# Kernel tuning notes

Measured on AMD Instinct MI355X. Metric: run time of the kernel, lower is better.

## Reference

```python
import jax, jax.numpy as jnp
import numpy as np

N_POINTS = 262144
NUM_LEVELS = 16
LEVEL_DIM = 8
BASE_RES = 16
LOG2_HASH = 21
BOUNDS = 10.0
TEXT_REP = 512
IMAGE_REP = 512
MLP_WIDTH = 256
PRIMES = (1, 2654435761, 805459861)  # instant-NGP fast_hash primes


def _level_layout():
    # mirrors torch-ngp GridEncoder offset computation
    max_params = 2 ** LOG2_HASH
    sizes, offsets = [], [0]
    for l in range(NUM_LEVELS):
        res = int(np.ceil(BASE_RES * (2.0 ** l)))
        p = min(max_params, res ** 3)
        p = int(np.ceil(p / 8) * 8)  # align to 8
        sizes.append(p)
        offsets.append(offsets[-1] + p)
    return sizes, offsets

SIZES, OFFSETS = _level_layout()
TOTAL_PARAMS = OFFSETS[-1]  # ~27.56M rows


def grid_encode(u, embeddings):
    """u: [N,3] in [0,1]; torch-ngp kernel remaps with bound=1: u=(u+1)/2.
    With this config (res+1)^3 > hashmap_size at every level, so the hash
    path is always taken (faithful to get_grid_index)."""
    u = (u + 1.0) * 0.5
    feats = []
    for l in range(NUM_LEVELS):
        scale = 2.0 ** l * BASE_RES - 1.0          # exp2(l*log2(s))*H - 1
        pos = u * scale + 0.5                       # align_corners=False
        base = jnp.floor(pos)
        frac = pos - base                           # [N,3] trilinear fracs
        pg = base.astype(jnp.uint32)
        acc = jnp.zeros((u.shape[0], LEVEL_DIM), dtype=u.dtype)
        for corner in range(8):
            bits = [(corner >> d) & 1 for d in range(3)]
            cpos = pg + jnp.asarray(bits, dtype=jnp.uint32)
            w = jnp.prod(jnp.where(jnp.asarray(bits, dtype=bool), frac, 1.0 - frac), axis=-1)
            h = (cpos[:, 0] * jnp.uint32(PRIMES[0])
                 ^ cpos[:, 1] * jnp.uint32(PRIMES[1])
                 ^ cpos[:, 2] * jnp.uint32(PRIMES[2]))  # uint32 wraparound hash
            idx = (h % jnp.uint32(SIZES[l])).astype(jnp.int32) + OFFSETS[l]
            acc = acc + w[:, None] * embeddings[idx]    # gather [N,8]
        feats.append(acc)
    return jnp.concatenate(feats, axis=-1)              # [N, 128]


def setup_inputs() -> dict:
    key = jax.random.key(0)
    ks = jax.random.split(key, 8)
    x = jax.random.uniform(ks[0], (N_POINTS, 3), jnp.float32, -BOUNDS, BOUNDS)
    emb = jax.random.uniform(ks[1], (TOTAL_PARAMS, LEVEL_DIM), jnp.float32, -1e-4, 1e-4)
    d_in = NUM_LEVELS * LEVEL_DIM  # 128
    d_out = TEXT_REP + IMAGE_REP   # 1024
    W1 = jax.random.normal(ks[2], (d_in, MLP_WIDTH), jnp.float32) * (1.0 / np.sqrt(d_in))
    b1 = jnp.zeros((MLP_WIDTH,), jnp.float32)
    W2 = jax.random.normal(ks[3], (MLP_WIDTH, MLP_WIDTH), jnp.float32) * (1.0 / np.sqrt(MLP_WIDTH))
    b2 = jnp.zeros((MLP_WIDTH,), jnp.float32)
    W3 = jax.random.normal(ks[4], (MLP_WIDTH, d_out), jnp.float32) * (1.0 / np.sqrt(MLP_WIDTH))
    b3 = jnp.zeros((d_out,), jnp.float32)
    return {"x": x, "embeddings": emb, "W1": W1, "b1": b1, "W2": W2, "b2": b2, "W3": W3, "b3": b3}


def reference(x, embeddings, W1, b1, W2, b2, W3, b3):
    # bound normalization: (x - min) / (max - min), min=-10, max=+10
    bounded = (x + BOUNDS) / (2.0 * BOUNDS)
    gh = grid_encode(bounded, embeddings)
    h = jax.nn.relu(gh @ W1 + b1)
    h = jax.nn.relu(h @ W2 + b2)
    out = h @ W3 + b3
    label_latent = out[..., :TEXT_REP]
    image_latent = out[..., TEXT_REP:TEXT_REP + IMAGE_REP]  # image head = Identity
    return (label_latent, image_latent)
```

## Files before the change

### kernel.cpp

```cpp
#include <hip/hip_runtime.h>
#include <cstdint>

#pragma STDC FP_CONTRACT OFF


typedef _Float16 f16;
typedef __attribute__((ext_vector_type(8))) _Float16 f16x8;
typedef __attribute__((ext_vector_type(4))) float f32x4;

#define ACT_SCALE 4096.0f
#define INV_ACT_SCALE (1.0f / 4096.0f)

__device__ __forceinline__ void gld16(const void* g, void* l) {
  __builtin_amdgcn_global_load_lds(
      (const __attribute__((address_space(1))) void*)(uintptr_t)g,
      (__attribute__((address_space(3))) void*)(uint32_t)(uintptr_t)l,
      16, 0, 0);
}

__global__ __launch_bounds__(256) void grid_encode_kernel(
    const float* __restrict__ x, const float* __restrict__ emb,
    f16* __restrict__ gh, int p0, int npts)
{
#pragma clang fp contract(off)
  int g = blockIdx.x * blockDim.x + threadIdx.x;
  if (g >= npts * 16) return;
  int pl = g >> 4;
  int l  = g & 15;
  int p  = p0 + pl;

  float x0 = x[3 * p + 0];
  float x1 = x[3 * p + 1];
  float x2 = x[3 * p + 2];

  float t0 = (x0 + 10.0f) * 0.05f;
  float t1 = (x1 + 10.0f) * 0.05f;
  float t2 = (x2 + 10.0f) * 0.05f;
  asm volatile("" : "+v"(t0), "+v"(t1), "+v"(t2));
  float u0 = (t0 + 1.0f) * 0.5f;
  float u1 = (t1 + 1.0f) * 0.5f;
  float u2 = (t2 + 1.0f) * 0.5f;
  asm volatile("" : "+v"(u0), "+v"(u1), "+v"(u2));

  float scale = (float)((16 << l) - 1);
  float pos0 = u0 * scale + 0.5f;
  float pos1 = u1 * scale + 0.5f;
  float pos2 = u2 * scale + 0.5f;

  float fb0 = floorf(pos0), fb1 = floorf(pos1), fb2 = floorf(pos2);
  float f0 = pos0 - fb0;
  float f1 = pos1 - fb1;
  float f2 = pos2 - fb2;
  uint32_t px = (uint32_t)fb0, py = (uint32_t)fb1, pz = (uint32_t)fb2;

  uint32_t mask = (l < 3) ? ((4096u << (3 * l)) - 1u) : 2097151u;
  uint32_t off;
  if (l == 0)      off = 0u;
  else if (l == 1) off = 4096u;
  else if (l == 2) off = 36864u;
  else             off = 299008u + (uint32_t)(l - 3) * 2097152u;

  float wx[2] = {1.0f - f0, f0};
  float wy[2] = {1.0f - f1, f1};
  float wz[2] = {1.0f - f2, f2};

  float acc[8];
#pragma unroll
  for (int j = 0; j < 8; ++j) acc[j] = 0.0f;

#pragma unroll
  for (int c = 0; c < 8; ++c) {
    uint32_t cx = px + (uint32_t)(c & 1);
    uint32_t cy = py + (uint32_t)((c >> 1) & 1);
    uint32_t cz = pz + (uint32_t)((c >> 2) & 1);
    float w = wx[c & 1] * wy[(c >> 1) & 1] * wz[(c >> 2) & 1];
    uint32_t h = cx ^ (cy * 2654435761u) ^ (cz * 805459861u);
    uint32_t idx = (h & mask) + off;
    const float4* e = (const float4*)(emb + (size_t)idx * 8);
    float4 e0 = e[0];
    float4 e1 = e[1];
    float m0 = w * e0.x, m1 = w * e0.y, m2 = w * e0.z, m3 = w * e0.w;
    float m4 = w * e1.x, m5 = w * e1.y, m6 = w * e1.z, m7 = w * e1.w;
    asm volatile("" : "+v"(m0), "+v"(m1), "+v"(m2), "+v"(m3),
                      "+v"(m4), "+v"(m5), "+v"(m6), "+v"(m7));
    acc[0] += m0; acc[1] += m1; acc[2] += m2; acc[3] += m3;
    acc[4] += m4; acc[5] += m5; acc[6] += m6; acc[7] += m7;
  }

  f16x8 o;
#pragma unroll
  for (int j = 0; j < 8; ++j) o[j] = (f16)(acc[j] * ACT_SCALE);
  *(f16x8*)&gh[(size_t)pl * 128 + l * 8] = o;
}

template <int K, int N>
__global__ __launch_bounds__(256) void prep_w(
    const float* __restrict__ W, f16* __restrict__ Wt)
{
  int i = blockIdx.x * 256 + threadIdx.x;
  if (i >= N * K) return;
  int n = i / K, k = i - n * K;
  Wt[i] = (f16)W[(size_t)k * N + n];
}

__global__ __launch_bounds__(256) void prep_w2f(
    const float* __restrict__ W2, f16* __restrict__ Wf2)
{
  int i = blockIdx.x * 256 + threadIdx.x;
  if (i >= 256 * 256) return;
  int e  = i & 7;
  int lr = (i >> 3) & 15;
  int kg = (i >> 7) & 31;
  int q  = i >> 12;
  int n = q * 16 + lr;
  int k = kg * 8 + e;
  Wf2[i] = (f16)W2[(size_t)k * 256 + n];
}

template <int K, int N>
__global__ __launch_bounds__(256) void mfma_gemm1(
    const f16* __restrict__ A, const f16* __restrict__ Wt,
    const float* __restrict__ bias, f16* __restrict__ Cout)
{
  constexpr int BM = 128, BK = 64, KT = K / BK;
  __shared__ alignas(16) f16 As[2][BM * BK];
  __shared__ alignas(16) f16 Bs[2][BM * BK];

  const int tid  = threadIdx.x;
  const int lane = tid & 63;
  const int wid  = tid >> 6;
  const int wr   = wid >> 1;
  const int wc   = wid & 1;
  const int bm   = blockIdx.x * BM;
  const int bn   = blockIdx.y * BM;

  const int lr  = lane & 15;
  const int lkg = lane >> 4;

  f32x4 acc[4][4];
#pragma unroll
  for (int i = 0; i < 4; ++i)
#pragma unroll
    for (int j = 0; j < 4; ++j) acc[i][j] = (f32x4){0.f, 0.f, 0.f, 0.f};

  const int srow_off = lane >> 3;
  const int sg       = lane & 7;

  auto stage = [&](int buf, int kt) {
#pragma unroll
    for (int i = 0; i < 4; ++i) {
      const int r0  = wid * 32 + i * 8;
      const int row = r0 + srow_off;
      const int gs  = sg ^ (row & 7);
      gld16(&A[(size_t)(bm + row) * K + kt * BK + gs * 8], &As[buf][r0 * BK]);
      gld16(&Wt[(size_t)(bn + row) * K + kt * BK + gs * 8], &Bs[buf][r0 * BK]);
    }
  };

  stage(0, 0);
  __syncthreads();

  for (int kt = 0; kt < KT; ++kt) {
    const int cur = kt & 1;
    if (kt + 1 < KT) stage(cur ^ 1, kt + 1);
#pragma unroll
    for (int kk = 0; kk < 2; ++kk) {
      f16x8 af[4], bf[4];
#pragma unroll
      for (int i = 0; i < 4; ++i) {
        const int ar = wr * 64 + i * 16 + lr;
        const int br = wc * 64 + i * 16 + lr;
        af[i] = *(const f16x8*)&As[cur][ar * BK + ((kk * 4 + lkg) ^ (ar & 7)) * 8];
        bf[i] = *(const f16x8*)&Bs[cur][br * BK + ((kk * 4 + lkg) ^ (br & 7)) * 8];
      }
#pragma unroll
      for (int i = 0; i < 4; ++i)
#pragma unroll
        for (int j = 0; j < 4; ++j)
          acc[i][j] = __builtin_amdgcn_mfma_f32_16x16x32_f16(
              af[i], bf[j], acc[i][j], 0, 0, 0);
    }
    __syncthreads();
  }

  const int orow0 = bm + wr * 64;
  const int ocol0 = bn + wc * 64;
#pragma unroll
  for (int i = 0; i < 4; ++i)
#pragma unroll
    for (int j = 0; j < 4; ++j) {
      int col = ocol0 + j * 16 + lr;
      float bv = bias[col];
#pragma unroll
      for (int q = 0; q < 4; ++q) {
        int row = orow0 + i * 16 + lkg * 4 + q;
        float v = fmaxf(acc[i][j][q] + bv * ACT_SCALE, 0.0f);
        Cout[(size_t)row * N + col] = (f16)v;
      }
    }
}

__global__ __launch_bounds__(512) void fused_gemm23(
    const f16* __restrict__ h1, const f16* __restrict__ Wf2,
    const float* __restrict__ b2, const f16* __restrict__ Wt3,
    const float* __restrict__ b3, float* __restrict__ out,
    int rowBase, int nTotal)
{
  constexpr int K1 = 256;
  __shared__ alignas(16) f16 As2[2][8192];
  __shared__ alignas(16) f16 H2[128 * 256];

  const int tid  = threadIdx.x;
  const int lane = tid & 63;
  const int wid  = tid >> 6;
  const int bm   = blockIdx.x * 128;
  const int lr   = lane & 15;
  const int lkg  = lane >> 4;

  const int rowg = wid >> 2;
  const int colg = wid & 3;

  f16x8 bf_all[4][8];
#pragma unroll
  for (int j = 0; j < 4; ++j)
#pragma unroll
    for (int f = 0; f < 8; ++f)
      bf_all[j][f] = *(const f16x8*)&Wf2[(((colg * 4 + j) * 32 + f * 4 + lkg) * 16 + lr) * 8];

  auto stage2 = [&](int buf, int kt) {
#pragma unroll
    for (int s = 0; s < 2; ++s) {
      const int gbase = wid * 64 + s * 512;
      const int g     = gbase + lane;
      const int row   = g >> 3;
      const int gs    = (g & 7) ^ (row & 7);
      gld16(&h1[(size_t)(bm + row) * K1 + kt * 64 + gs * 8],
            &As2[buf][gbase * 8]);
    }
  };

  f32x4 acc[4][4];
#pragma unroll
  for (int i = 0; i < 4; ++i)
#pragma unroll
    for (int j = 0; j < 4; ++j) acc[i][j] = (f32x4){0.f, 0.f, 0.f, 0.f};

  stage2(0, 0);
  __syncthreads();

#pragma unroll
  for (int kt = 0; kt < 4; ++kt) {
    const int cur = kt & 1;
    if (kt + 1 < 4) stage2(cur ^ 1, kt + 1);
#pragma unroll
    for (int kk = 0; kk < 2; ++kk) {
      f16x8 af[4];
#pragma unroll
      for (int i = 0; i < 4; ++i) {
        const int ar = rowg * 64 + i * 16 + lr;
        af[i] = *(const f16x8*)&As2[cur][ar * 64 + ((kk * 4 + lkg) ^ (ar & 7)) * 8];
      }
#pragma unroll
      for (int i = 0; i < 4; ++i)
#pragma unroll
        for (int j = 0; j < 4; ++j)
          acc[i][j] = __builtin_amdgcn_mfma_f32_16x16x32_f16(
              af[i], bf_all[j][kt * 2 + kk], acc[i][j], 0, 0, 0);
    }
    __syncthreads();
  }

#pragma unroll
  for (int i = 0; i < 4; ++i)
#pragma unroll
    for (int j = 0; j < 4; ++j) {
      const int col = colg * 64 + j * 16 + lr;
      const float bv = b2[col];
      const int kg = col >> 3, e = col & 7;
#pragma unroll
      for (int q = 0; q < 4; ++q) {
        const int row = rowg * 64 + i * 16 + lkg * 4 + q;
        const int kgs = (kg & 24) | ((kg ^ row) & 7);
        float v = fmaxf(acc[i][j][q] + bv * ACT_SCALE, 0.0f);
        H2[row * 256 + kgs * 8 + e] = (f16)v;
      }
    }

  const int rowg3 = wid & 3;
  const int colg3 = wid >> 2;

  auto stage3 = [&](int buf, int c) {
#pragma unroll
    for (int s = 0; s < 2; ++s) {
      const int gbase = wid * 64 + s * 512;
      const int g     = gbase + lane;
      const int row   = g >> 5;
      const int sg    = g & 31;
      const int gs    = (sg & 24) | ((sg ^ row) & 7);
      gld16(&Wt3[(size_t)(c * 32 + row) * 256 + gs * 8],
            &As2[buf][gbase * 8]);
    }
  };

  stage3(0, 0);
  __syncthreads();

  f16x8 af3[2][8];
#pragma unroll
  for (int i = 0; i < 2; ++i)
#pragma unroll
    for (int f = 0; f < 8; ++f) {
      const int r  = rowg3 * 32 + i * 16 + lr;
      const int kg = f * 4 + lkg;
      const int kgs = (kg & 24) | ((kg ^ r) & 7);
      af3[i][f] = *(const f16x8*)&H2[r * 256 + kgs * 8];
    }

  for (int c = 0; c < 32; ++c) {
    const int buf = c & 1;
    if (c + 1 < 32) stage3(buf ^ 1, c + 1);

    f16x8 bf3[8];
#pragma unroll
    for (int f = 0; f < 8; ++f) {
      const int n  = colg3 * 16 + lr;
      const int kg = f * 4 + lkg;
      const int kgs = (kg & 24) | ((kg ^ n) & 7);
      bf3[f] = *(const f16x8*)&As2[buf][n * 256 + kgs * 8];
    }

    f32x4 a3[2];
#pragma unroll
    for (int i = 0; i < 2; ++i) {
      a3[i] = (f32x4){0.f, 0.f, 0.f, 0.f};
#pragma unroll
      for (int f = 0; f < 8; ++f)
        a3[i] = __builtin_amdgcn_mfma_f32_16x16x32_f16(af3[i][f], bf3[f], a3[i], 0, 0, 0);
    }

    const int col = c * 32 + colg3 * 16 + lr;
    const float bv = b3[col];
#pragma unroll
    for (int i = 0; i < 2; ++i) {
#pragma unroll
      for (int q = 0; q < 4; ++q) {
        const int row = bm + rowg3 * 32 + i * 16 + lkg * 4 + q;
        float v = a3[i][q] * INV_ACT_SCALE + bv;
        size_t grow = (size_t)(rowBase + row);
        float* dst = (col < 512)
                         ? (out + grow * 512 + col)
                         : (out + (size_t)nTotal * 512 + grow * 512 + (col - 512));
        *dst = v;
      }
    }
    __syncthreads();
  }
}

extern "C" void kernel_launch(void* const* d_in, const int* in_sizes, int n_in,
                              void* d_out, int out_size, void* d_ws, size_t ws_size,
                              hipStream_t stream)
{
  const float* x   = (const float*)d_in[0];
  const float* emb = (const float*)d_in[1];
  const float* W1  = (const float*)d_in[2];
  const float* b1  = (const float*)d_in[3];
  const float* W2  = (const float*)d_in[4];
  const float* b2  = (const float*)d_in[5];
  const float* W3  = (const float*)d_in[6];
  const float* b3  = (const float*)d_in[7];
  float* out = (float*)d_out;

  const int NPTS = in_sizes[0] / 3;

  f16* Wt1 = (f16*)d_ws;
  f16* Wf2 = Wt1 + 128 * 256;
  f16* Wt3 = Wf2 + 256 * 256;
  f16* wsAct = Wt3 + 256 * 1024;
  const size_t wtBytes = (size_t)(128 * 256 + 256 * 256 + 256 * 1024) * sizeof(f16);

  long long cmax = (long long)((ws_size - wtBytes) / 768);
  int C = (int)((cmax / 128) * 128);
  if (C > NPTS) C = NPTS;
  if (C < 128) C = 128;

  f16* gh = wsAct;
  f16* h1 = gh + (size_t)C * 128;

  prep_w<128, 256><<<(128 * 256 + 255) / 256, 256, 0, stream>>>(W1, Wt1);
  prep_w2f<<<(256 * 256 + 255) / 256, 256, 0, stream>>>(W2, Wf2);
  prep_w<256, 1024><<<(256 * 1024 + 255) / 256, 256, 0, stream>>>(W3, Wt3);

  for (int p0 = 0; p0 < NPTS; p0 += C) {
    int cur = (NPTS - p0 < C) ? (NPTS - p0) : C;

    int nthr = cur * 16;
    grid_encode_kernel<<<(nthr + 255) / 256, 256, 0, stream>>>(x, emb, gh, p0, cur);

    dim3 g1(cur / 128, 2);
    mfma_gemm1<128, 256><<<g1, 256, 0, stream>>>(gh, Wt1, b1, h1);

    fused_gemm23<<<cur / 128, 512, 0, stream>>>(h1, Wf2, b2, Wt3, b3, out, p0, NPTS);
  }
}
```

Before: 867.6 us.

## Fuse first MLP layer into fused GEMM kernel, keep h1 in LDS

Removes the separate mfma_gemm1 kernel and its h1 round trip through global memory by computing layer 1 inside the fused MLP kernel, staging the grid features into LDS and keeping h1 in shared memory. W1 is pre-swizzled into a fragment layout loaded straight into registers. The layer-3 loop is reshaped so each wave owns 16 rows over 64 column chunks of 16, with a two-deep prefetch of W3 tiles. LDS use rises to about 144 KB per block, which may limit occupancy, and the per-chunk sync pattern changes.

```diff
diff --git a/kernel.cpp b/kernel.cpp
--- a/kernel.cpp
+++ b/kernel.cpp
@@ -103,6 +103,20 @@
   Wt[i] = (f16)W[(size_t)k * N + n];
 }
 
+__global__ __launch_bounds__(256) void prep_w1f(
+    const float* __restrict__ W1, f16* __restrict__ Wf1)
+{
+  int i = blockIdx.x * 256 + threadIdx.x;
+  if (i >= 128 * 256) return;
+  int e  = i & 7;
+  int lr = (i >> 3) & 15;
+  int kg = (i >> 7) & 15;
+  int q  = i >> 11;
+  int n = q * 16 + lr;
+  int k = kg * 8 + e;
+  Wf1[i] = (f16)W1[(size_t)k * 256 + n];
+}
+
 __global__ __launch_bounds__(256) void prep_w2f(
     const float* __restrict__ W2, f16* __restrict__ Wf2)
 {
@@ -117,97 +131,15 @@
   Wf2[i] = (f16)W2[(size_t)k * 256 + n];
 }
 
-template <int K, int N>
-__global__ __launch_bounds__(256) void mfma_gemm1(
-    const f16* __restrict__ A, const f16* __restrict__ Wt,
-    const float* __restrict__ bias, f16* __restrict__ Cout)
-{
-  constexpr int BM = 128, BK = 64, KT = K / BK;
-  __shared__ alignas(16) f16 As[2][BM * BK];
-  __shared__ alignas(16) f16 Bs[2][BM * BK];
-
-  const int tid  = threadIdx.x;
-  const int lane = tid & 63;
-  const int wid  = tid >> 6;
-  const int wr   = wid >> 1;
-  const int wc   = wid & 1;
-  const int bm   = blockIdx.x * BM;
-  const int bn   = blockIdx.y * BM;
-
-  const int lr  = lane & 15;
-  const int lkg = lane >> 4;
-
-  f32x4 acc[4][4];
-#pragma unroll
-  for (int i = 0; i < 4; ++i)
-#pragma unroll
-    for (int j = 0; j < 4; ++j) acc[i][j] = (f32x4){0.f, 0.f, 0.f, 0.f};
-
-  const int srow_off = lane >> 3;
-  const int sg       = lane & 7;
-
-  auto stage = [&](int buf, int kt) {
-#pragma unroll
-    for (int i = 0; i < 4; ++i) {
-      const int r0  = wid * 32 + i * 8;
-      const int row = r0 + srow_off;
-      const int gs  = sg ^ (row & 7);
-      gld16(&A[(size_t)(bm + row) * K + kt * BK + gs * 8], &As[buf][r0 * BK]);
-      gld16(&Wt[(size_t)(bn + row) * K + kt * BK + gs * 8], &Bs[buf][r0 * BK]);
-    }
-  };
-
-  stage(0, 0);
-  __syncthreads();
-
-  for (int kt = 0; kt < KT; ++kt) {
-    const int cur = kt & 1;
-    if (kt + 1 < KT) stage(cur ^ 1, kt + 1);
-#pragma unroll
-    for (int kk = 0; kk < 2; ++kk) {
-      f16x8 af[4], bf[4];
-#pragma unroll
-      for (int i = 0; i < 4; ++i) {
-        const int ar = wr * 64 + i * 16 + lr;
-        const int br = wc * 64 + i * 16 + lr;
-        af[i] = *(const f16x8*)&As[cur][ar * BK + ((kk * 4 + lkg) ^ (ar & 7)) * 8];
-        bf[i] = *(const f16x8*)&Bs[cur][br * BK + ((kk * 4 + lkg) ^ (br & 7)) * 8];
-      }
-#pragma unroll
-      for (int i = 0; i < 4; ++i)
-#pragma unroll
-        for (int j = 0; j < 4; ++j)
-          acc[i][j] = __builtin_amdgcn_mfma_f32_16x16x32_f16(
-              af[i], bf[j], acc[i][j], 0, 0, 0);
-    }
-    __syncthreads();
-  }
-
-  const int orow0 = bm + wr * 64;
-  const int ocol0 = bn + wc * 64;
-#pragma unroll
-  for (int i = 0; i < 4; ++i)
-#pragma unroll
-    for (int j = 0; j < 4; ++j) {
-      int col = ocol0 + j * 16 + lr;
-      float bv = bias[col];
-#pragma unroll
-      for (int q = 0; q < 4; ++q) {
-        int row = orow0 + i * 16 + lkg * 4 + q;
-        float v = fmaxf(acc[i][j][q] + bv * ACT_SCALE, 0.0f);
-        Cout[(size_t)row * N + col] = (f16)v;
-      }
-    }
-}
-
-__global__ __launch_bounds__(512) void fused_gemm23(
-    const f16* __restrict__ h1, const f16* __restrict__ Wf2,
+__global__ __launch_bounds__(512) void fused_mlp(
+    const f16* __restrict__ gh, const f16* __restrict__ Wf1,
+    const float* __restrict__ b1, const f16* __restrict__ Wf2,
     const float* __restrict__ b2, const f16* __restrict__ Wt3,
     const float* __restrict__ b3, float* __restrict__ out,
     int rowBase, int nTotal)
 {
-  constexpr int K1 = 256;
-  __shared__ alignas(16) f16 As2[2][8192];
+  __shared__ alignas(16) f16 As2[2][4096];
+  __shared__ alignas(16) f16 H1[128 * 256];
   __shared__ alignas(16) f16 H2[128 * 256];
 
   const int tid  = threadIdx.x;
@@ -217,143 +149,165 @@
   const int lr   = lane & 15;
   const int lkg  = lane >> 4;
 
-  const int rowg = wid >> 2;
-  const int colg = wid & 3;
-
-  f16x8 bf_all[4][8];
-#pragma unroll
-  for (int j = 0; j < 4; ++j)
-#pragma unroll
-    for (int f = 0; f < 8; ++f)
-      bf_all[j][f] = *(const f16x8*)&Wf2[(((colg * 4 + j) * 32 + f * 4 + lkg) * 16 + lr) * 8];
-
-  auto stage2 = [&](int buf, int kt) {
-#pragma unroll
-    for (int s = 0; s < 2; ++s) {
-      const int gbase = wid * 64 + s * 512;
-      const int g     = gbase + lane;
-      const int row   = g >> 3;
-      const int gs    = (g & 7) ^ (row & 7);
-      gld16(&h1[(size_t)(bm + row) * K1 + kt * 64 + gs * 8],
-            &As2[buf][gbase * 8]);
-    }
+  auto stage3 = [&](int buf, int c) {
+    const int g   = tid;
+    const int row = g >> 5;
+    const int sg  = g & 31;
+    const int gs  = (sg & 24) | ((sg ^ row) & 7);
+    gld16(&Wt3[(size_t)(c * 16 + row) * 256 + gs * 8], &As2[buf][g * 8]);
   };
 
-  f32x4 acc[4][4];
-#pragma unroll
-  for (int i = 0; i < 4; ++i)
-#pragma unroll
-    for (int j = 0; j < 4; ++j) acc[i][j] = (f32x4){0.f, 0.f, 0.f, 0.f};
-
-  stage2(0, 0);
+#pragma unroll
+  for (int s = 0; s < 4; ++s) {
+    const int g   = tid + s * 512;
+    const int row = g >> 4;
+    const int sg  = g & 15;
+    const int gs  = (sg & 8) | ((sg ^ row) & 7);
+    gld16(&gh[(size_t)(bm + row) * 128 + gs * 8], &H2[g * 8]);
+  }
+  stage3(0, 0);
+  stage3(1, 1);
   __syncthreads();
 
-#pragma unroll
-  for (int kt = 0; kt < 4; ++kt) {
-    const int cur = kt & 1;
-    if (kt + 1 < 4) stage2(cur ^ 1, kt + 1);
-#pragma unroll
-    for (int kk = 0; kk < 2; ++kk) {
+  {
+    const int rowg = wid >> 2, colg = wid & 3;
+    f16x8 bf1[4][4];
+#pragma unroll
+    for (int j = 0; j < 4; ++j)
+#pragma unroll
+      for (int f = 0; f < 4; ++f)
+        bf1[j][f] = *(const f16x8*)&Wf1[(((colg * 4 + j) * 16 + f * 4 + lkg) * 16 + lr) * 8];
+
+    f32x4 acc[4][4];
+#pragma unroll
+    for (int i = 0; i < 4; ++i)
+#pragma unroll
+      for (int j = 0; j < 4; ++j) acc[i][j] = (f32x4){0.f, 0.f, 0.f, 0.f};
+
+#pragma unroll
+    for (int f = 0; f < 4; ++f) {
       f16x8 af[4];
 #pragma unroll
       for (int i = 0; i < 4; ++i) {
-        const int ar = rowg * 64 + i * 16 + lr;
-        af[i] = *(const f16x8*)&As2[cur][ar * 64 + ((kk * 4 + lkg) ^ (ar & 7)) * 8];
+        const int r  = rowg * 64 + i * 16 + lr;
+        const int kg = f * 4 + lkg;
+        const int gs = (kg & 8) | ((kg ^ r) & 7);
+        af[i] = *(const f16x8*)&H2[r * 128 + gs * 8];
       }
 #pragma unroll
       for (int i = 0; i < 4; ++i)
 #pragma unroll
         for (int j = 0; j < 4; ++j)
           acc[i][j] = __builtin_amdgcn_mfma_f32_16x16x32_f16(
-              af[i], bf_all[j][kt * 2 + kk], acc[i][j], 0, 0, 0);
+              af[i], bf1[j][f], acc[i][j], 0, 0, 0);
+    }
+
+#pragma unroll
+    for (int i = 0; i < 4; ++i)
+#pragma unroll
+      for (int j = 0; j < 4; ++j) {
+        const int col = colg * 64 + j * 16 + lr;
+        const float bv = b1[col];
+        const int kg = col >> 3, e = col & 7;
+#pragma unroll
+        for (int q = 0; q < 4; ++q) {
+          const int row = rowg * 64 + i * 16 + lkg * 4 + q;
+          const int kgs = (kg & 24) | ((kg ^ row) & 7);
+          float v = fmaxf(acc[i][j][q] + bv * ACT_SCALE, 0.0f);
+          H1[row * 256 + kgs * 8 + e] = (f16)v;
+        }
+      }
+  }
+  __syncthreads();
+
+  {
+    const int rowg = wid >> 2, colg = wid & 3;
+    f16x8 bf2[4][8];
+#pragma unroll
+    for (int j = 0; j < 4; ++j)
+#pragma unroll
+      for (int f = 0; f < 8; ++f)
+        bf2[j][f] = *(const f16x8*)&Wf2[(((colg * 4 + j) * 32 + f * 4 + lkg) * 16 + lr) * 8];
+
+    f32x4 acc[4][4];
+#pragma unroll
+    for (int i = 0; i < 4; ++i)
+#pragma unroll
+      for (int j = 0; j < 4; ++j) acc[i][j] = (f32x4){0.f, 0.f, 0.f, 0.f};
+
+#pragma unroll
+    for (int f = 0; f < 8; ++f) {
+      f16x8 af[4];
+#pragma unroll
+      for (int i = 0; i < 4; ++i) {
+        const int r   = rowg * 64 + i * 16 + lr;
+        const int kg  = f * 4 + lkg;
+        const int kgs = (kg & 24) | ((kg ^ r) & 7);
+        af[i] = *(const f16x8*)&H1[r * 256 + kgs * 8];
+      }
+#pragma unroll
+      for (int i = 0; i < 4; ++i)
+#pragma unroll
+        for (int j = 0; j < 4; ++j)
+          acc[i][j] = __builtin_amdgcn_mfma_f32_16x16x32_f16(
+              af[i], bf2[j][f], acc[i][j], 0, 0, 0);
+    }
+
+#pragma unroll
+    for (int i = 0; i < 4; ++i)
+#pragma unroll
+      for (int j = 0; j < 4; ++j) {
+        const int col = colg * 64 + j * 16 + lr;
+        const float bv = b2[col];
+        const int kg = col >> 3, e = col & 7;
+#pragma unroll
+        for (int q = 0; q < 4; ++q) {
+          const int row = rowg * 64 + i * 16 + lkg * 4 + q;
+          const int kgs = (kg & 24) | ((kg ^ row) & 7);
+          float v = fmaxf(acc[i][j][q] + bv * ACT_SCALE, 0.0f);
+          H2[row * 256 + kgs * 8 + e] = (f16)v;
+        }
+      }
+  }
+  __syncthreads();
+
+  f16x8 af3[8];
+#pragma unroll
+  for (int f = 0; f < 8; ++f) {
+    const int r   = wid * 16 + lr;
+    const int kg  = f * 4 + lkg;
+    const int kgs = (kg & 24) | ((kg ^ r) & 7);
+    af3[f] = *(const f16x8*)&H2[r * 256 + kgs * 8];
+  }
+
+  for (int c = 0; c < 64; ++c) {
+    const int buf = c & 1;
+    f16x8 bf3[8];
+#pragma unroll
+    for (int f = 0; f < 8; ++f) {
+      const int kg  = f * 4 + lkg;
+      const int kgs = (kg & 24) | ((kg ^ lr) & 7);
+      bf3[f] = *(const f16x8*)&As2[buf][(lr * 32 + kgs) * 8];
+    }
+    f32x4 a = (f32x4){0.f, 0.f, 0.f, 0.f};
+#pragma unroll
+    for (int f = 0; f < 8; ++f)
+      a = __builtin_amdgcn_mfma_f32_16x16x32_f16(af3[f], bf3[f], a, 0, 0, 0);
+
+    const int col = c * 16 + lr;
+    const float bv = b3[col];
+#pragma unroll
+    for (int q = 0; q < 4; ++q) {
+      const int row = bm + wid * 16 + lkg * 4 + q;
+      float v = a[q] * INV_ACT_SCALE + bv;
+      size_t grow = (size_t)(rowBase + row);
+      float* dst = (col < 512)
+                       ? (out + grow * 512 + col)
+                       : (out + (size_t)nTotal * 512 + grow * 512 + (col - 512));
+      *dst = v;
     }
     __syncthreads();
-  }
-
-#pragma unroll
-  for (int i = 0; i < 4; ++i)
-#pragma unroll
-    for (int j = 0; j < 4; ++j) {
-      const int col = colg * 64 + j * 16 + lr;
-      const float bv = b2[col];
-      const int kg = col >> 3, e = col & 7;
-#pragma unroll
-      for (int q = 0; q < 4; ++q) {
-        const int row = rowg * 64 + i * 16 + lkg * 4 + q;
-        const int kgs = (kg & 24) | ((kg ^ row) & 7);
-        float v = fmaxf(acc[i][j][q] + bv * ACT_SCALE, 0.0f);
-        H2[row * 256 + kgs * 8 + e] = (f16)v;
-      }
-    }
-
-  const int rowg3 = wid & 3;
-  const int colg3 = wid >> 2;
-
-  auto stage3 = [&](int buf, int c) {
-#pragma unroll
-    for (int s = 0; s < 2; ++s) {
-      const int gbase = wid * 64 + s * 512;
-      const int g     = gbase + lane;
-      const int row   = g >> 5;
-      const int sg    = g & 31;
-      const int gs    = (sg & 24) | ((sg ^ row) & 7);
-      gld16(&Wt3[(size_t)(c * 32 + row) * 256 + gs * 8],
-            &As2[buf][gbase * 8]);
-    }
-  };
-
-  stage3(0, 0);
-  __syncthreads();
-
-  f16x8 af3[2][8];
-#pragma unroll
-  for (int i = 0; i < 2; ++i)
-#pragma unroll
-    for (int f = 0; f < 8; ++f) {
-      const int r  = rowg3 * 32 + i * 16 + lr;
-      const int kg = f * 4 + lkg;
-      const int kgs = (kg & 24) | ((kg ^ r) & 7);
-      af3[i][f] = *(const f16x8*)&H2[r * 256 + kgs * 8];
-    }
-
-  for (int c = 0; c < 32; ++c) {
-    const int buf = c & 1;
-    if (c + 1 < 32) stage3(buf ^ 1, c + 1);
-
-    f16x8 bf3[8];
-#pragma unroll
-    for (int f = 0; f < 8; ++f) {
-      const int n  = colg3 * 16 + lr;
-      const int kg = f * 4 + lkg;
-      const int kgs = (kg & 24) | ((kg ^ n) & 7);
-      bf3[f] = *(const f16x8*)&As2[buf][n * 256 + kgs * 8];
-    }
-
-    f32x4 a3[2];
-#pragma unroll
-    for (int i = 0; i < 2; ++i) {
-      a3[i] = (f32x4){0.f, 0.f, 0.f, 0.f};
-#pragma unroll
-      for (int f = 0; f < 8; ++f)
-        a3[i] = __builtin_amdgcn_mfma_f32_16x16x32_f16(af3[i][f], bf3[f], a3[i], 0, 0, 0);
-    }
-
-    const int col = c * 32 + colg3 * 16 + lr;
-    const float bv = b3[col];
-#pragma unroll
-    for (int i = 0; i < 2; ++i) {
-#pragma unroll
-      for (int q = 0; q < 4; ++q) {
-        const int row = bm + rowg3 * 32 + i * 16 + lkg * 4 + q;
-        float v = a3[i][q] * INV_ACT_SCALE + bv;
-        size_t grow = (size_t)(rowBase + row);
-        float* dst = (col < 512)
-                         ? (out + grow * 512 + col)
-                         : (out + (size_t)nTotal * 512 + grow * 512 + (col - 512));
-        *dst = v;
-      }
-    }
-    __syncthreads();
+    if (c + 2 < 64) stage3(buf, c + 2);
   }
 }
 
@@ -373,21 +327,18 @@
 
   const int NPTS = in_sizes[0] / 3;
 
-  f16* Wt1 = (f16*)d_ws;
-  f16* Wf2 = Wt1 + 128 * 256;
+  f16* Wf1 = (f16*)d_ws;
+  f16* Wf2 = Wf1 + 128 * 256;
   f16* Wt3 = Wf2 + 256 * 256;
-  f16* wsAct = Wt3 + 256 * 1024;
+  f16* gh0 = Wt3 + 256 * 1024;
   const size_t wtBytes = (size_t)(128 * 256 + 256 * 256 + 256 * 1024) * sizeof(f16);
 
-  long long cmax = (long long)((ws_size - wtBytes) / 768);
+  long long cmax = (long long)((ws_size - wtBytes) / 256);
   int C = (int)((cmax / 128) * 128);
   if (C > NPTS) C = NPTS;
   if (C < 128) C = 128;
 
-  f16* gh = wsAct;
-  f16* h1 = gh + (size_t)C * 128;
-
-  prep_w<128, 256><<<(128 * 256 + 255) / 256, 256, 0, stream>>>(W1, Wt1);
+  prep_w1f<<<(128 * 256 + 255) / 256, 256, 0, stream>>>(W1, Wf1);
   prep_w2f<<<(256 * 256 + 255) / 256, 256, 0, stream>>>(W2, Wf2);
   prep_w<256, 1024><<<(256 * 1024 + 255) / 256, 256, 0, stream>>>(W3, Wt3);
 
@@ -395,11 +346,9 @@
     int cur = (NPTS - p0 < C) ? (NPTS - p0) : C;
 
     int nthr = cur * 16;
-    grid_encode_kernel<<<(nthr + 255) / 256, 256, 0, stream>>>(x, emb, gh, p0, cur);
-
-    dim3 g1(cur / 128, 2);
-    mfma_gemm1<128, 256><<<g1, 256, 0, stream>>>(gh, Wt1, b1, h1);
-
-    fused_gemm23<<<cur / 128, 512, 0, stream>>>(h1, Wf2, b2, Wt3, b3, out, p0, NPTS);
-  }
-}
+    grid_encode_kernel<<<(nthr + 255) / 256, 256, 0, stream>>>(x, emb, gh0, p0, cur);
+
+    fused_mlp<<<cur / 128, 512, 0, stream>>>(gh0, Wf1, b1, Wf2, b2, Wt3, b3,
+                                             out, p0, NPTS);
+  }
+}
```

Result: no change. 881.4 us (+1.6%).
